# Performance work log

Measured on AMD Instinct MI355X. Metric: run time of the kernel, lower is better.

## Reference

```python
import jax, jax.numpy as jnp
import numpy as np

SCALE = 8      # scale_factor from map_to_mat_info
PATCH = 32     # up_delta - low_delta + 1 == right_delta - left_delta + 1 (uniform interior patches)


def setup_inputs() -> dict:
    key = jax.random.key(0)
    mat_h, mat_w = 160, 160
    H = (mat_h - 1) * SCALE + PATCH  # 1304: deltas (0,31,0,31) -> no border clipping
    W = (mat_w - 1) * SCALE + PATCH
    x = jax.random.normal(key, (1, 3, H, W), dtype=jnp.float32)
    rgb_weight = jnp.array([0.299, 0.587, 0.114], dtype=jnp.float32).reshape(1, 3, 1, 1)
    return {"x": x, "rgb_weight": rgb_weight, "mat_h": mat_h, "mat_w": mat_w}


def reference(x, rgb_weight, mat_h, mat_w):
    P = PATCH
    # RGB -> grayscale (convert_gray branch for in_channels == 3)
    gray = jnp.sum(x * rgb_weight, axis=1)[0]  # (H, W)
    # Gather all overlapping PxP patches at stride SCALE -> (mat_h, mat_w, P, P)
    rows = (jnp.arange(mat_h) * SCALE)[:, None] + jnp.arange(P)[None, :]  # (mat_h, P)
    cols = (jnp.arange(mat_w) * SCALE)[:, None] + jnp.arange(P)[None, :]  # (mat_w, P)
    p = gray[rows.reshape(-1)].reshape(mat_h, P, -1)              # (mat_h, P, W)
    p = p[:, :, cols.reshape(-1)].reshape(mat_h, P, mat_w, P)     # (mat_h, P, mat_w, P)
    patches = jnp.transpose(p, (0, 2, 1, 3))                      # (mat_h, mat_w, P, P)
    # torch.rfft(signal_ndim=2, onesided=False) == full 2D FFT; power = re^2 + im^2
    F = jnp.fft.fft2(patches)
    log_power = jnp.log(F.real * F.real + F.imag * F.imag + 1.0)
    # High-frequency region sums (h == w == P, static)
    lo = P // 2 - P // 4 - 1   # 7
    up = P // 2 + P // 4       # 24
    r1 = jnp.sum(log_power[..., lo:up + 1, :], axis=(-2, -1))
    r2 = jnp.sum(log_power[..., up + 1:, lo:up + 1], axis=(-2, -1))
    r3 = jnp.sum(log_power[..., :lo, lo:up + 1], axis=(-2, -1))
    mat = (r1 + r2 + r3)[None, None]  # (1, 1, mat_h, mat_w)
    return mat / jnp.max(mat)
```

## Files before the change

### kernel.cpp

```cpp
#include <hip/hip_runtime.h>
#include <math.h>

#define SCALE 8
#define PSZ 32

#define RSTRIDE 92
#define SSTRIDE (17 * RSTRIDE)

__device__ constexpr float C32[16] = {
     1.000000000000000f,  0.980785280403230f,  0.923879532511287f,  0.831469612302545f,
     0.707106781186548f,  0.555570233019602f,  0.382683432365090f,  0.195090322016128f,
     0.000000000000000f, -0.195090322016128f, -0.382683432365090f, -0.555570233019602f,
    -0.707106781186548f, -0.831469612302545f, -0.923879532511287f, -0.980785280403230f };
__device__ constexpr float S32[16] = {
     0.000000000000000f,  0.195090322016128f,  0.382683432365090f,  0.555570233019602f,
     0.707106781186548f,  0.831469612302545f,  0.923879532511287f,  0.980785280403230f,
     1.000000000000000f,  0.980785280403230f,  0.923879532511287f,  0.831469612302545f,
     0.707106781186548f,  0.555570233019602f,  0.382683432365090f,  0.195090322016128f };

__device__ __forceinline__ constexpr int brev4(int i) {
    return ((i & 1) << 3) | ((i & 2) << 1) | ((i & 4) >> 1) | ((i & 8) >> 3);
}

__device__ __forceinline__ void fft16(float re[16], float im[16]) {
#pragma unroll
    for (int i = 0; i < 16; ++i) {
        const int j = brev4(i);
        if (j > i) {
            float t = re[i]; re[i] = re[j]; re[j] = t;
            t = im[i]; im[i] = im[j]; im[j] = t;
        }
    }
#pragma unroll
    for (int s = 1; s <= 4; ++s) {
        const int m = 1 << s;
        const int h = m >> 1;
        const int tstep = 32 >> s;
#pragma unroll
        for (int k = 0; k < 16; k += m) {
#pragma unroll
            for (int j = 0; j < h; ++j) {
                const float wr = C32[j * tstep];
                const float wi = -S32[j * tstep];
                const int a = k + j;
                const int b = k + j + h;
                const float tr = wr * re[b] - wi * im[b];
                const float ti = wr * im[b] + wi * re[b];
                re[b] = re[a] - tr; im[b] = im[a] - ti;
                re[a] = re[a] + tr; im[a] = im[a] + ti;
            }
        }
    }
}

__device__ __forceinline__ unsigned pack_bf2(float hi, float lo) {
    const unsigned uh = __float_as_uint(hi) + 0x8000u;
    const unsigned ul = __float_as_uint(lo) + 0x8000u;
    return (uh & 0xFFFF0000u) | (ul >> 16);
}
__device__ __forceinline__ float bf_hi(unsigned u) { return __uint_as_float(u & 0xFFFF0000u); }
__device__ __forceinline__ float bf_lo(unsigned u) { return __uint_as_float(u << 16); }

__global__ __launch_bounds__(256) void gray_kernel(
        const float* __restrict__ x, const float* __restrict__ w,
        float* __restrict__ g, int n4, long long HW) {
    const int i = blockIdx.x * 256 + threadIdx.x;
    if (i >= n4) return;
    const float w0 = w[0], w1 = w[1], w2 = w[2];
    const float4 a = reinterpret_cast<const float4*>(x)[i];
    const float4 b = reinterpret_cast<const float4*>(x + HW)[i];
    const float4 c = reinterpret_cast<const float4*>(x + 2 * HW)[i];
    float4 o;
    o.x = w0 * a.x + w1 * b.x + w2 * c.x;
    o.y = w0 * a.y + w1 * b.y + w2 * c.y;
    o.z = w0 * a.z + w1 * b.z + w2 * c.z;
    o.w = w0 * a.w + w1 * b.w + w2 * c.w;
    reinterpret_cast<float4*>(g)[i] = o;
}

__global__ __launch_bounds__(256) void hfdft_tile_kernel(
        const float* __restrict__ g, float* __restrict__ out,
        float* __restrict__ partial, int W, int mat_w) {
    __shared__ unsigned spec[2 * SSTRIDE];
    __shared__ float red[16];

    const int tid = threadIdx.x;
    const int row0 = blockIdx.y * 64;
    const int col0 = blockIdx.x * 16;

    const bool is_even = (tid < 88);
    const bool is_odd = (tid >= 128 && tid < 216);
    if (is_even || is_odd) {
        const int y = is_even ? tid : (tid - 128);
        const float4* g4 = reinterpret_cast<const float4*>(
            g + (size_t)(row0 + y) * W + col0);
        float win[40];
#pragma unroll
        for (int q = 0; q < 10; ++q) {
            const float4 v = g4[q];
            win[4 * q + 0] = v.x; win[4 * q + 1] = v.y;
            win[4 * q + 2] = v.z; win[4 * q + 3] = v.w;
        }

        unsigned* sA = spec + y;
        unsigned* sB = spec + SSTRIDE + y;

        float fr[16], fi[16];
        if (is_even) {
#pragma unroll
            for (int i = 0; i < 16; ++i) {
                fr[i] = win[i] + win[i + 16];
                fi[i] = win[i + 8] + win[i + 24];
            }
            fft16(fr, fi);
            sA[0] = pack_bf2(fr[0], fr[8]);
            sB[0] = pack_bf2(fi[0], fi[8]);
#pragma unroll
            for (int k2 = 1; k2 <= 7; ++k2) {
                const int e2 = 16 - k2;
                const float far_ = 0.5f * (fr[k2] + fr[e2]);
                const float fai_ = 0.5f * (fi[k2] - fi[e2]);
                const float fbr_ = 0.5f * (fi[k2] + fi[e2]);
                const float fbi_ = 0.5f * (fr[e2] - fr[k2]);
                sA[(2 * k2) * RSTRIDE] = pack_bf2(far_, fai_);
                sB[(2 * k2) * RSTRIDE] = pack_bf2(fbr_, fbi_);
            }
        } else {
#pragma unroll
            for (int i = 0; i < 16; ++i) {
                const float dre = win[i] - win[i + 16];
                const float dim = win[i + 8] - win[i + 24];
                fr[i] = dre * C32[i] + dim * S32[i];
                fi[i] = dim * C32[i] - dre * S32[i];
            }
            fft16(fr, fi);
#pragma unroll
            for (int k2 = 0; k2 <= 7; ++k2) {
                const int o2 = 15 - k2;
                const float far_ = 0.5f * (fr[k2] + fr[o2]);
                const float fai_ = 0.5f * (fi[k2] - fi[o2]);
                const float fbr_ = 0.5f * (fi[k2] + fi[o2]);
                const float fbi_ = 0.5f * (fr[o2] - fr[k2]);
                sA[(2 * k2 + 1) * RSTRIDE] = pack_bf2(far_, fai_);
                sB[(2 * k2 + 1) * RSTRIDE] = pack_bf2(fbr_, fbi_);
            }
        }
    }

    __syncthreads();

    {
        const int pl = tid >> 4;
        const int slot = tid & 15;
        const int ph = pl >> 1, strip = pl & 1;
        const float b1f = (slot >= 7) ? 1.0f : 0.0f;
        const float m1f = (slot >= 8) ? 1.0f : 0.0f;

        unsigned u[32];
        {
            const uint4* p4 = reinterpret_cast<const uint4*>(
                spec + strip * SSTRIDE + slot * RSTRIDE + ph * 8);
#pragma unroll
            for (int q = 0; q < 8; ++q) {
                const uint4 v = p4[q];
                u[4 * q + 0] = v.x; u[4 * q + 1] = v.y;
                u[4 * q + 2] = v.z; u[4 * q + 3] = v.w;
            }
        }

        float s0 = 0.0f, s1 = 0.0f;

        {
            float er[16], ei[16];
#pragma unroll
            for (int i = 0; i < 16; ++i) {
                er[i] = bf_hi(u[i]) + bf_hi(u[i + 16]);
                ei[i] = bf_lo(u[i]) + bf_lo(u[i + 16]);
            }
            fft16(er, ei);
            if (slot == 0) {
#pragma unroll
                for (int k2 = 0; k2 <= 8; ++k2) {
                    const int kr = 2 * k2;
                    const int b = (k2 == 0) ? 0 : 16 - k2;
                    const float g0r = 0.5f * (er[k2] + er[b]);
                    const float g0i = 0.5f * (ei[k2] - ei[b]);
                    const float g1r = 0.5f * (ei[k2] + ei[b]);
                    const float g1i = 0.5f * (er[b] - er[k2]);
                    const float w0c = (kr >= 7 ? 1.0f : 0.0f) + ((kr >= 8 && kr <= 15) ? 1.0f : 0.0f);
                    const float w16c = 1.0f + ((kr >= 1 && kr <= 15) ? 1.0f : 0.0f);
                    if (w0c > 0.0f)
                        s0 = fmaf(w0c, __logf(g0r * g0r + g0i * g0i + 1.0f), s0);
                    s1 = fmaf(w16c, __logf(g1r * g1r + g1i * g1i + 1.0f), s1);
                }
            } else {
#pragma unroll
                for (int k2 = 0; k2 < 16; ++k2) {
                    const int kr = 2 * k2;
                    const float lp = __logf(er[k2] * er[k2] + ei[k2] * ei[k2] + 1.0f);
                    const float wgt = (kr >= 8 && kr <= 24) ? 2.0f : (b1f + m1f);
                    if (k2 & 1) s1 = fmaf(wgt, lp, s1);
                    else        s0 = fmaf(wgt, lp, s0);
                }
            }
        }

        {
            float orr[16], oi[16];
#pragma unroll
            for (int i = 0; i < 16; ++i) {
                const float dre = bf_hi(u[i]) - bf_hi(u[i + 16]);
                const float dim = bf_lo(u[i]) - bf_lo(u[i + 16]);
                orr[i] = dre * C32[i] + dim * S32[i];
                oi[i]  = dim * C32[i] - dre * S32[i];
            }
            fft16(orr, oi);
            if (slot == 0) {
#pragma unroll
                for (int k2 = 0; k2 <= 7; ++k2) {
                    const int kr = 2 * k2 + 1;
                    const int b = 15 - k2;
                    const float g0r = 0.5f * (orr[k2] + orr[b]);
                    const float g0i = 0.5f * (oi[k2] - oi[b]);
                    const float g1r = 0.5f * (oi[k2] + oi[b]);
                    const float g1i = 0.5f * (orr[b] - orr[k2]);
                    const float w0c = (kr >= 7 ? 1.0f : 0.0f) + ((kr >= 8 && kr <= 15) ? 1.0f : 0.0f);
                    const float w16c = 2.0f;
                    if (w0c > 0.0f)
                        s0 = fmaf(w0c, __logf(g0r * g0r + g0i * g0i + 1.0f), s0);
                    s1 = fmaf(w16c, __logf(g1r * g1r + g1i * g1i + 1.0f), s1);
                }
            } else {
#pragma unroll
                for (int k2 = 0; k2 < 16; ++k2) {
                    const int kr = 2 * k2 + 1;
                    const float lp = __logf(orr[k2] * orr[k2] + oi[k2] * oi[k2] + 1.0f);
                    float wgt;
                    if (kr == 7)                   wgt = 1.0f + m1f;
                    else if (kr == 25)             wgt = b1f + 1.0f;
                    else if (kr >= 9 && kr <= 23)  wgt = 2.0f;
                    else                           wgt = b1f + m1f;
                    if (k2 & 1) s1 = fmaf(wgt, lp, s1);
                    else        s0 = fmaf(wgt, lp, s0);
                }
            }
        }

        float s = s0 + s1;
#pragma unroll
        for (int off = 8; off >= 1; off >>= 1) s += __shfl_xor(s, off, 16);
        if (slot == 0) {
            out[(blockIdx.y * 8 + ph) * mat_w + blockIdx.x * 2 + strip] = s;
            red[pl] = s;
        }
    }

    __syncthreads();

    if (tid == 0) {
        float m = red[0];
#pragma unroll
        for (int i = 1; i < 16; ++i) m = fmaxf(m, red[i]);
        partial[blockIdx.y * gridDim.x + blockIdx.x] = m;
    }
}

template <bool GRAY_PRE>
__global__ __launch_bounds__(128) void hfdft_patch_kernel(
        const float* __restrict__ x, const float* __restrict__ w,
        float* __restrict__ out, int H, int W, int mat_h, int mat_w) {
    __shared__ unsigned cb[4 * 528];
    __shared__ float red[8];

    const int tid = threadIdx.x;
    const int h = tid >> 6;
    const int lane = tid & 63;
    const int total = mat_h * mat_w;
    const long long HW = (long long)H * W;
    const int Pbase = blockIdx.x * 4;

    {
        const int g = lane >> 5, r = lane & 31;
        int pA = Pbase + 2 * g;
        if (pA > total - 1) pA = total - 1;
        int pB = pA + 1; if (pB > total - 1) pB = total - 1;
        const int phA = pA / mat_w, pwA = pA % mat_w;
        const int phB = pB / mat_w, pwB = pB % mat_w;
        const bool adj = (phA == phB) && (pwB == pwA + 1);
        const int baseA = (phA * SCALE + r) * W + pwA * SCALE;
        const int baseB = (phB * SCALE + r) * W + pwB * SCALE;

        float ar[32], br[32];
        if (GRAY_PRE && adj) {
            float win[40];
            const float4* g4 = reinterpret_cast<const float4*>(x + baseA);
#pragma unroll
            for (int q = 0; q < 10; ++q) {
                const float4 v = g4[q];
                win[4 * q + 0] = v.x; win[4 * q + 1] = v.y;
                win[4 * q + 2] = v.z; win[4 * q + 3] = v.w;
            }
#pragma unroll
            for (int i = 0; i < 32; ++i) { ar[i] = win[i]; br[i] = win[i + 8]; }
        } else if (GRAY_PRE) {
#pragma unroll
            for (int i = 0; i < 32; ++i) { ar[i] = x[baseA + i]; br[i] = x[baseB + i]; }
        } else {
            const float w0 = w[0], w1 = w[1], w2 = w[2];
#pragma unroll
            for (int i = 0; i < 32; ++i) {
                ar[i] = w0 * x[baseA + i] + w1 * x[HW + baseA + i] + w2 * x[2 * HW + baseA + i];
                br[i] = w0 * x[baseB + i] + w1 * x[HW + baseB + i] + w2 * x[2 * HW + baseB + i];
            }
        }

        float fr[16], fi[16];
        if (h == 0) {
#pragma unroll
            for (int i = 0; i < 16; ++i) {
                fr[i] = ar[i] + ar[i + 16];
                fi[i] = br[i] + br[i + 16];
            }
        } else {
#pragma unroll
            for (int i = 0; i < 16; ++i) {
                const float dre = ar[i] - ar[i + 16];
                const float dim = br[i] - br[i + 16];
                fr[i] = dre * C32[i] + dim * S32[i];
                fi[i] = dim * C32[i] - dre * S32[i];
            }
        }

        fft16(fr, fi);

        unsigned* cbA = cb + (2 * g) * 528;
        unsigned* cbB = cbA + 528;
        if (h == 0) {
            cbA[r] = pack_bf2(fr[0], fr[8]);
            cbB[r] = pack_bf2(fi[0], fi[8]);
#pragma unroll
            for (int k2 = 1; k2 <= 7; ++k2) {
                const int e2 = 16 - k2;
                const float far_ = 0.5f * (fr[k2] + fr[e2]);
                const float fai_ = 0.5f * (fi[k2] - fi[e2]);
                const float fbr_ = 0.5f * (fi[k2] + fi[e2]);
                const float fbi_ = 0.5f * (fr[e2] - fr[k2]);
                cbA[(2 * k2) * 33 + r] = pack_bf2(far_, fai_);
                cbB[(2 * k2) * 33 + r] = pack_bf2(fbr_, fbi_);
            }
        } else {
#pragma unroll
            for (int k2 = 0; k2 <= 7; ++k2) {
                const int o2 = 15 - k2;
                const float far_ = 0.5f * (fr[k2] + fr[o2]);
                const float fai_ = 0.5f * (fi[k2] - fi[o2]);
                const float fbr_ = 0.5f * (fi[k2] + fi[o2]);
                const float fbi_ = 0.5f * (fr[o2] - fr[k2]);
                cbA[(2 * k2 + 1) * 33 + r] = pack_bf2(far_, fai_);
                cbB[(2 * k2 + 1) * 33 + r] = pack_bf2(fbr_, fbi_);
            }
        }
    }

    __syncthreads();

    {
        const int pl = lane >> 4, slot = lane & 15;
        int p = Pbase + pl;
        if (p > total - 1) p = total - 1;
        const unsigned* cbp = cb + pl * 528 + slot * 33;

        float fr[16], fi[16];
        if (h == 0) {
#pragma unroll
            for (int i = 0; i < 16; ++i) {
                const unsigned u0 = cbp[i], u1 = cbp[i + 16];
                fr[i] = bf_hi(u0) + bf_hi(u1);
                fi[i] = bf_lo(u0) + bf_lo(u1);
            }
        } else {
#pragma unroll
            for (int i = 0; i < 16; ++i) {
                const unsigned u0 = cbp[i], u1 = cbp[i + 16];
                const float dre = bf_hi(u0) - bf_hi(u1);
                const float dim = bf_lo(u0) - bf_lo(u1);
                fr[i] = dre * C32[i] + dim * S32[i];
                fi[i] = dim * C32[i] - dre * S32[i];
            }
        }

        fft16(fr, fi);

        float s0 = 0.0f, s1 = 0.0f;
        if (slot == 0) {
            if (h == 0) {
#pragma unroll
                for (int k2 = 0; k2 <= 8; ++k2) {
                    const int kr = 2 * k2;
                    const int b = (k2 == 0) ? 0 : 16 - k2;
                    const float g0r = 0.5f * (fr[k2] + fr[b]);
                    const float g0i = 0.5f * (fi[k2] - fi[b]);
                    const float g1r = 0.5f * (fi[k2] + fi[b]);
                    const float g1i = 0.5f * (fr[b] - fr[k2]);
                    const float w0c = (kr >= 7 ? 1.0f : 0.0f) + ((kr >= 8 && kr <= 15) ? 1.0f : 0.0f);
                    const float w16c = 1.0f + ((kr >= 1 && kr <= 15) ? 1.0f : 0.0f);
                    if (w0c > 0.0f)
                        s0 = fmaf(w0c, __logf(g0r * g0r + g0i * g0i + 1.0f), s0);
                    s1 = fmaf(w16c, __logf(g1r * g1r + g1i * g1i + 1.0f), s1);
                }
            } else {
#pragma unroll
                for (int k2 = 0; k2 <= 7; ++k2) {
                    const int kr = 2 * k2 + 1;
                    const int b = 15 - k2;
                    const float g0r = 0.5f * (fr[k2] + fr[b]);
                    const float g0i = 0.5f * (fi[k2] - fi[b]);
                    const float g1r = 0.5f * (fi[k2] + fi[b]);
                    const float g1i = 0.5f * (fr[b] - fr[k2]);
                    const float w0c = (kr >= 7 ? 1.0f : 0.0f) + ((kr >= 8 && kr <= 15) ? 1.0f : 0.0f);
                    const float w16c = 2.0f;
                    if (w0c > 0.0f)
                        s0 = fmaf(w0c, __logf(g0r * g0r + g0i * g0i + 1.0f), s0);
                    s1 = fmaf(w16c, __logf(g1r * g1r + g1i * g1i + 1.0f), s1);
                }
            }
        } else {
            const float b1f = (slot >= 7) ? 1.0f : 0.0f;
            const float m1f = (slot >= 8) ? 1.0f : 0.0f;
            if (h == 0) {
#pragma unroll
                for (int k2 = 0; k2 < 16; ++k2) {
                    const int kr = 2 * k2;
                    const float lp = __logf(fr[k2] * fr[k2] + fi[k2] * fi[k2] + 1.0f);
                    const float wgt = (kr >= 8 && kr <= 24) ? 2.0f : (b1f + m1f);
                    if (k2 & 1) s1 = fmaf(wgt, lp, s1);
                    else        s0 = fmaf(wgt, lp, s0);
                }
            } else {
#pragma unroll
                for (int k2 = 0; k2 < 16; ++k2) {
                    const int kr = 2 * k2 + 1;
                    const float lp = __logf(fr[k2] * fr[k2] + fi[k2] * fi[k2] + 1.0f);
                    float wgt;
                    if (kr == 7)                   wgt = 1.0f + m1f;
                    else if (kr == 25)             wgt = b1f + 1.0f;
                    else if (kr >= 9 && kr <= 23)  wgt = 2.0f;
                    else                           wgt = b1f + m1f;
                    if (k2 & 1) s1 = fmaf(wgt, lp, s1);
                    else        s0 = fmaf(wgt, lp, s0);
                }
            }
        }

        float s = s0 + s1;
#pragma unroll
        for (int off = 8; off >= 1; off >>= 1) s += __shfl_xor(s, off, 16);
        if (slot == 0) red[pl * 2 + h] = s;
    }

    __syncthreads();

    if (tid < 4) {
        const int p = Pbase + tid;
        if (p < total) out[p] = red[tid * 2] + red[tid * 2 + 1];
    }
}

__global__ __launch_bounds__(1024) void max_kernel(
        const float* __restrict__ sums, int n, float* __restrict__ partial) {
    __shared__ float sm[16];
    float m = 0.0f;
    for (int i = blockIdx.x * 1024 + threadIdx.x; i < n; i += gridDim.x * 1024)
        m = fmaxf(m, sums[i]);
#pragma unroll
    for (int off = 32; off >= 1; off >>= 1) m = fmaxf(m, __shfl_xor(m, off, 64));
    if ((threadIdx.x & 63) == 0) sm[threadIdx.x >> 6] = m;
    __syncthreads();
    if (threadIdx.x == 0) {
#pragma unroll
        for (int i = 1; i < 16; ++i) m = fmaxf(m, sm[i]);
        partial[blockIdx.x] = m;
    }
}

__global__ __launch_bounds__(256) void norm_kernel(
        float* __restrict__ out, int n,
        const float* __restrict__ partial, int np) {
    __shared__ float sm[4];
    float m = 0.0f;
    for (int i = threadIdx.x; i < np; i += 256) m = fmaxf(m, partial[i]);
#pragma unroll
    for (int off = 32; off >= 1; off >>= 1) m = fmaxf(m, __shfl_xor(m, off, 64));
    if ((threadIdx.x & 63) == 0) sm[threadIdx.x >> 6] = m;
    __syncthreads();
    m = fmaxf(fmaxf(sm[0], sm[1]), fmaxf(sm[2], sm[3]));
    const int i = blockIdx.x * 256 + threadIdx.x;
    if (i < n) out[i] = out[i] / m;
}

extern "C" void kernel_launch(void* const* d_in, const int* in_sizes, int n_in,
                              void* d_out, int out_size, void* d_ws, size_t ws_size,
                              hipStream_t stream) {
    const float* x = (const float*)d_in[0];
    const float* w = (const float*)d_in[1];
    float* out = (float*)d_out;

    const int HWi = in_sizes[0] / 3;
    const int H = (int)(sqrt((double)HWi) + 0.5);
    const int W = H;
    const long long HW = (long long)H * W;
    const int mat = (int)(sqrt((double)out_size) + 0.5);
    const int total = mat * mat;

    float* partial = (float*)d_ws;
    float* gray = (float*)((char*)d_ws + 8192);
    const int nparts = (mat / 2) * (mat / 8);
    const size_t need = 8192 + (size_t)HW * 4;

    const bool shape_ok = ((mat & 7) == 0) && (W == (mat - 1) * SCALE + PSZ)
                          && (H == W) && ((W & 3) == 0)
                          && ws_size >= need && (size_t)nparts * 4 <= 8192;

    if (shape_ok) {
        const int n4 = (int)(HW / 4);
        hipLaunchKernelGGL(gray_kernel, dim3((n4 + 255) / 256), dim3(256), 0, stream,
                           x, w, gray, n4, HW);
        dim3 gridT(mat / 2, mat / 8);
        hipLaunchKernelGGL(hfdft_tile_kernel, gridT, dim3(256), 0, stream,
                           gray, out, partial, W, mat);
        hipLaunchKernelGGL(norm_kernel, dim3((total + 255) / 256), dim3(256), 0, stream,
                           out, total, partial, nparts);
    } else if (ws_size >= need && (W & 3) == 0) {
        const int n4 = (int)(HW / 4);
        hipLaunchKernelGGL(gray_kernel, dim3((n4 + 255) / 256), dim3(256), 0, stream,
                           x, w, gray, n4, HW);
        hipLaunchKernelGGL((hfdft_patch_kernel<true>), dim3((total + 3) / 4), dim3(128), 0, stream,
                           gray, w, out, H, W, mat, mat);
        hipLaunchKernelGGL(max_kernel, dim3(8), dim3(1024), 0, stream, out, total, partial);
        hipLaunchKernelGGL(norm_kernel, dim3((total + 255) / 256), dim3(256), 0, stream,
                           out, total, partial, 8);
    } else {
        hipLaunchKernelGGL((hfdft_patch_kernel<false>), dim3((total + 3) / 4), dim3(128), 0, stream,
                           x, w, out, H, W, mat, mat);
        hipLaunchKernelGGL(max_kernel, dim3(8), dim3(1024), 0, stream, out, total, partial);
        hipLaunchKernelGGL(norm_kernel, dim3((total + 255) / 256), dim3(256), 0, stream,
                           out, total, partial, 8);
    }
}
```

Before: 43.71 us.

## Fuse grayscale conversion into tile kernel via shared-memory window staging

```diff
diff --git a/kernel.cpp b/kernel.cpp
--- a/kernel.cpp
+++ b/kernel.cpp
@@ -4,6 +4,7 @@
 #define SCALE 8
 #define PSZ 32
 
+#define WSTRIDE 41
 #define RSTRIDE 92
 #define SSTRIDE (17 * RSTRIDE)
 
@@ -60,6 +61,212 @@
 }
 __device__ __forceinline__ float bf_hi(unsigned u) { return __uint_as_float(u & 0xFFFF0000u); }
 __device__ __forceinline__ float bf_lo(unsigned u) { return __uint_as_float(u << 16); }
+
+__global__ __launch_bounds__(256) void hfdft_tile_kernel(
+        const float* __restrict__ x, const float* __restrict__ w,
+        float* __restrict__ out, float* __restrict__ partial,
+        int W, int mat_w, long long HW) {
+    __shared__ float win[88 * WSTRIDE];
+    __shared__ unsigned spec[2 * SSTRIDE];
+    __shared__ float red[16];
+
+    const int tid = threadIdx.x;
+    const int row0 = blockIdx.y * 64;
+    const int col0 = blockIdx.x * 16;
+
+    {
+        const float w0 = w[0], w1 = w[1], w2 = w[2];
+        for (int idx = tid; idx < 880; idx += 256) {
+            const int row = idx / 10;
+            const int f4 = idx - row * 10;
+            const float* base = x + (size_t)(row0 + row) * W + col0 + f4 * 4;
+            const float4 a = *reinterpret_cast<const float4*>(base);
+            const float4 b = *reinterpret_cast<const float4*>(base + HW);
+            const float4 c = *reinterpret_cast<const float4*>(base + 2 * HW);
+            float* wp = win + row * WSTRIDE + f4 * 4;
+            wp[0] = w0 * a.x + w1 * b.x + w2 * c.x;
+            wp[1] = w0 * a.y + w1 * b.y + w2 * c.y;
+            wp[2] = w0 * a.z + w1 * b.z + w2 * c.z;
+            wp[3] = w0 * a.w + w1 * b.w + w2 * c.w;
+        }
+    }
+
+    __syncthreads();
+
+    const bool is_even = (tid < 88);
+    const bool is_odd = (tid >= 128 && tid < 216);
+    if (is_even || is_odd) {
+        const int y = is_even ? tid : (tid - 128);
+        const float* wrow = win + y * WSTRIDE;
+
+        unsigned* sA = spec + y;
+        unsigned* sB = spec + SSTRIDE + y;
+
+        float fr[16], fi[16];
+        if (is_even) {
+#pragma unroll
+            for (int i = 0; i < 16; ++i) {
+                fr[i] = wrow[i] + wrow[i + 16];
+                fi[i] = wrow[i + 8] + wrow[i + 24];
+            }
+            fft16(fr, fi);
+            sA[0] = pack_bf2(fr[0], fr[8]);
+            sB[0] = pack_bf2(fi[0], fi[8]);
+#pragma unroll
+            for (int k2 = 1; k2 <= 7; ++k2) {
+                const int e2 = 16 - k2;
+                const float far_ = 0.5f * (fr[k2] + fr[e2]);
+                const float fai_ = 0.5f * (fi[k2] - fi[e2]);
+                const float fbr_ = 0.5f * (fi[k2] + fi[e2]);
+                const float fbi_ = 0.5f * (fr[e2] - fr[k2]);
+                sA[(2 * k2) * RSTRIDE] = pack_bf2(far_, fai_);
+                sB[(2 * k2) * RSTRIDE] = pack_bf2(fbr_, fbi_);
+            }
+        } else {
+#pragma unroll
+            for (int i = 0; i < 16; ++i) {
+                const float dre = wrow[i] - wrow[i + 16];
+                const float dim = wrow[i + 8] - wrow[i + 24];
+                fr[i] = dre * C32[i] + dim * S32[i];
+                fi[i] = dim * C32[i] - dre * S32[i];
+            }
+            fft16(fr, fi);
+#pragma unroll
+            for (int k2 = 0; k2 <= 7; ++k2) {
+                const int o2 = 15 - k2;
+                const float far_ = 0.5f * (fr[k2] + fr[o2]);
+                const float fai_ = 0.5f * (fi[k2] - fi[o2]);
+                const float fbr_ = 0.5f * (fi[k2] + fi[o2]);
+                const float fbi_ = 0.5f * (fr[o2] - fr[k2]);
+                sA[(2 * k2 + 1) * RSTRIDE] = pack_bf2(far_, fai_);
+                sB[(2 * k2 + 1) * RSTRIDE] = pack_bf2(fbr_, fbi_);
+            }
+        }
+    }
+
+    __syncthreads();
+
+    {
+        const int pl = tid >> 4;
+        const int slot = tid & 15;
+        const int ph = pl >> 1, strip = pl & 1;
+        const uint4* p4 = reinterpret_cast<const uint4*>(
+            spec + strip * SSTRIDE + slot * RSTRIDE + ph * 8);
+        const float b1f = (slot >= 7) ? 1.0f : 0.0f;
+        const float m1f = (slot >= 8) ? 1.0f : 0.0f;
+
+        float s0 = 0.0f, s1 = 0.0f;
+
+        {
+            float er[16], ei[16];
+#pragma unroll
+            for (int q = 0; q < 4; ++q) {
+                const uint4 lo = p4[q];
+                const uint4 hi = p4[q + 4];
+                er[4 * q + 0] = bf_hi(lo.x) + bf_hi(hi.x);
+                ei[4 * q + 0] = bf_lo(lo.x) + bf_lo(hi.x);
+                er[4 * q + 1] = bf_hi(lo.y) + bf_hi(hi.y);
+                ei[4 * q + 1] = bf_lo(lo.y) + bf_lo(hi.y);
+                er[4 * q + 2] = bf_hi(lo.z) + bf_hi(hi.z);
+                ei[4 * q + 2] = bf_lo(lo.z) + bf_lo(hi.z);
+                er[4 * q + 3] = bf_hi(lo.w) + bf_hi(hi.w);
+                ei[4 * q + 3] = bf_lo(lo.w) + bf_lo(hi.w);
+            }
+            fft16(er, ei);
+            if (slot == 0) {
+#pragma unroll
+                for (int k2 = 0; k2 <= 8; ++k2) {
+                    const int kr = 2 * k2;
+                    const int b = (k2 == 0) ? 0 : 16 - k2;
+                    const float g0r = 0.5f * (er[k2] + er[b]);
+                    const float g0i = 0.5f * (ei[k2] - ei[b]);
+                    const float g1r = 0.5f * (ei[k2] + ei[b]);
+                    const float g1i = 0.5f * (er[b] - er[k2]);
+                    const float w0c = (kr >= 7 ? 1.0f : 0.0f) + ((kr >= 8 && kr <= 15) ? 1.0f : 0.0f);
+                    const float w16c = 1.0f + ((kr >= 1 && kr <= 15) ? 1.0f : 0.0f);
+                    if (w0c > 0.0f)
+                        s0 = fmaf(w0c, __logf(g0r * g0r + g0i * g0i + 1.0f), s0);
+                    s1 = fmaf(w16c, __logf(g1r * g1r + g1i * g1i + 1.0f), s1);
+                }
+            } else {
+#pragma unroll
+                for (int k2 = 0; k2 < 16; ++k2) {
+                    const int kr = 2 * k2;
+                    const float lp = __logf(er[k2] * er[k2] + ei[k2] * ei[k2] + 1.0f);
+                    const float wgt = (kr >= 8 && kr <= 24) ? 2.0f : (b1f + m1f);
+                    if (k2 & 1) s1 = fmaf(wgt, lp, s1);
+                    else        s0 = fmaf(wgt, lp, s0);
+                }
+            }
+        }
+
+        {
+            float orr[16], oi[16];
+#pragma unroll
+            for (int q = 0; q < 4; ++q) {
+                const uint4 lo = p4[q];
+                const uint4 hi = p4[q + 4];
+#pragma unroll
+                for (int j = 0; j < 4; ++j) {
+                    const unsigned ul = (&lo.x)[j];
+                    const unsigned uh = (&hi.x)[j];
+                    const int i = 4 * q + j;
+                    const float dre = bf_hi(ul) - bf_hi(uh);
+                    const float dim = bf_lo(ul) - bf_lo(uh);
+                    orr[i] = dre * C32[i] + dim * S32[i];
+                    oi[i]  = dim * C32[i] - dre * S32[i];
+                }
+            }
+            fft16(orr, oi);
+            if (slot == 0) {
+#pragma unroll
+                for (int k2 = 0; k2 <= 7; ++k2) {
+                    const int kr = 2 * k2 + 1;
+                    const int b = 15 - k2;
+                    const float g0r = 0.5f * (orr[k2] + orr[b]);
+                    const float g0i = 0.5f * (oi[k2] - oi[b]);
+                    const float g1r = 0.5f * (oi[k2] + oi[b]);
+                    const float g1i = 0.5f * (orr[b] - orr[k2]);
+                    const float w0c = (kr >= 7 ? 1.0f : 0.0f) + ((kr >= 8 && kr <= 15) ? 1.0f : 0.0f);
+                    const float w16c = 2.0f;
+                    if (w0c > 0.0f)
+                        s0 = fmaf(w0c, __logf(g0r * g0r + g0i * g0i + 1.0f), s0);
+                    s1 = fmaf(w16c, __logf(g1r * g1r + g1i * g1i + 1.0f), s1);
+                }
+            } else {
+#pragma unroll
+                for (int k2 = 0; k2 < 16; ++k2) {
+                    const int kr = 2 * k2 + 1;
+                    const float lp = __logf(orr[k2] * orr[k2] + oi[k2] * oi[k2] + 1.0f);
+                    float wgt;
+                    if (kr == 7)                   wgt = 1.0f + m1f;
+                    else if (kr == 25)             wgt = b1f + 1.0f;
+                    else if (kr >= 9 && kr <= 23)  wgt = 2.0f;
+                    else                           wgt = b1f + m1f;
+                    if (k2 & 1) s1 = fmaf(wgt, lp, s1);
+                    else        s0 = fmaf(wgt, lp, s0);
+                }
+            }
+        }
+
+        float s = s0 + s1;
+#pragma unroll
+        for (int off = 8; off >= 1; off >>= 1) s += __shfl_xor(s, off, 16);
+        if (slot == 0) {
+            out[(blockIdx.y * 8 + ph) * mat_w + blockIdx.x * 2 + strip] = s;
+            red[pl] = s;
+        }
+    }
+
+    __syncthreads();
+
+    if (tid == 0) {
+        float m = red[0];
+#pragma unroll
+        for (int i = 1; i < 16; ++i) m = fmaxf(m, red[i]);
+        partial[blockIdx.y * gridDim.x + blockIdx.x] = m;
+    }
+}
 
 __global__ __launch_bounds__(256) void gray_kernel(
         const float* __restrict__ x, const float* __restrict__ w,
@@ -78,193 +285,6 @@
     reinterpret_cast<float4*>(g)[i] = o;
 }
 
-__global__ __launch_bounds__(256) void hfdft_tile_kernel(
-        const float* __restrict__ g, float* __restrict__ out,
-        float* __restrict__ partial, int W, int mat_w) {
-    __shared__ unsigned spec[2 * SSTRIDE];
-    __shared__ float red[16];
-
-    const int tid = threadIdx.x;
-    const int row0 = blockIdx.y * 64;
-    const int col0 = blockIdx.x * 16;
-
-    const bool is_even = (tid < 88);
-    const bool is_odd = (tid >= 128 && tid < 216);
-    if (is_even || is_odd) {
-        const int y = is_even ? tid : (tid - 128);
-        const float4* g4 = reinterpret_cast<const float4*>(
-            g + (size_t)(row0 + y) * W + col0);
-        float win[40];
-#pragma unroll
-        for (int q = 0; q < 10; ++q) {
-            const float4 v = g4[q];
-            win[4 * q + 0] = v.x; win[4 * q + 1] = v.y;
-            win[4 * q + 2] = v.z; win[4 * q + 3] = v.w;
-        }
-
-        unsigned* sA = spec + y;
-        unsigned* sB = spec + SSTRIDE + y;
-
-        float fr[16], fi[16];
-        if (is_even) {
-#pragma unroll
-            for (int i = 0; i < 16; ++i) {
-                fr[i] = win[i] + win[i + 16];
-                fi[i] = win[i + 8] + win[i + 24];
-            }
-            fft16(fr, fi);
-            sA[0] = pack_bf2(fr[0], fr[8]);
-            sB[0] = pack_bf2(fi[0], fi[8]);
-#pragma unroll
-            for (int k2 = 1; k2 <= 7; ++k2) {
-                const int e2 = 16 - k2;
-                const float far_ = 0.5f * (fr[k2] + fr[e2]);
-                const float fai_ = 0.5f * (fi[k2] - fi[e2]);
-                const float fbr_ = 0.5f * (fi[k2] + fi[e2]);
-                const float fbi_ = 0.5f * (fr[e2] - fr[k2]);
-                sA[(2 * k2) * RSTRIDE] = pack_bf2(far_, fai_);
-                sB[(2 * k2) * RSTRIDE] = pack_bf2(fbr_, fbi_);
-            }
-        } else {
-#pragma unroll
-            for (int i = 0; i < 16; ++i) {
-                const float dre = win[i] - win[i + 16];
-                const float dim = win[i + 8] - win[i + 24];
-                fr[i] = dre * C32[i] + dim * S32[i];
-                fi[i] = dim * C32[i] - dre * S32[i];
-            }
-            fft16(fr, fi);
-#pragma unroll
-            for (int k2 = 0; k2 <= 7; ++k2) {
-                const int o2 = 15 - k2;
-                const float far_ = 0.5f * (fr[k2] + fr[o2]);
-                const float fai_ = 0.5f * (fi[k2] - fi[o2]);
-                const float fbr_ = 0.5f * (fi[k2] + fi[o2]);
-                const float fbi_ = 0.5f * (fr[o2] - fr[k2]);
-                sA[(2 * k2 + 1) * RSTRIDE] = pack_bf2(far_, fai_);
-                sB[(2 * k2 + 1) * RSTRIDE] = pack_bf2(fbr_, fbi_);
-            }
-        }
-    }
-
-    __syncthreads();
-
-    {
-        const int pl = tid >> 4;
-        const int slot = tid & 15;
-        const int ph = pl >> 1, strip = pl & 1;
-        const float b1f = (slot >= 7) ? 1.0f : 0.0f;
-        const float m1f = (slot >= 8) ? 1.0f : 0.0f;
-
-        unsigned u[32];
-        {
-            const uint4* p4 = reinterpret_cast<const uint4*>(
-                spec + strip * SSTRIDE + slot * RSTRIDE + ph * 8);
-#pragma unroll
-            for (int q = 0; q < 8; ++q) {
-                const uint4 v = p4[q];
-                u[4 * q + 0] = v.x; u[4 * q + 1] = v.y;
-                u[4 * q + 2] = v.z; u[4 * q + 3] = v.w;
-            }
-        }
-
-        float s0 = 0.0f, s1 = 0.0f;
-
-        {
-            float er[16], ei[16];
-#pragma unroll
-            for (int i = 0; i < 16; ++i) {
-                er[i] = bf_hi(u[i]) + bf_hi(u[i + 16]);
-                ei[i] = bf_lo(u[i]) + bf_lo(u[i + 16]);
-            }
-            fft16(er, ei);
-            if (slot == 0) {
-#pragma unroll
-                for (int k2 = 0; k2 <= 8; ++k2) {
-                    const int kr = 2 * k2;
-                    const int b = (k2 == 0) ? 0 : 16 - k2;
-                    const float g0r = 0.5f * (er[k2] + er[b]);
-                    const float g0i = 0.5f * (ei[k2] - ei[b]);
-                    const float g1r = 0.5f * (ei[k2] + ei[b]);
-                    const float g1i = 0.5f * (er[b] - er[k2]);
-                    const float w0c = (kr >= 7 ? 1.0f : 0.0f) + ((kr >= 8 && kr <= 15) ? 1.0f : 0.0f);
-                    const float w16c = 1.0f + ((kr >= 1 && kr <= 15) ? 1.0f : 0.0f);
-                    if (w0c > 0.0f)
-                        s0 = fmaf(w0c, __logf(g0r * g0r + g0i * g0i + 1.0f), s0);
-                    s1 = fmaf(w16c, __logf(g1r * g1r + g1i * g1i + 1.0f), s1);
-                }
-            } else {
-#pragma unroll
-                for (int k2 = 0; k2 < 16; ++k2) {
-                    const int kr = 2 * k2;
-                    const float lp = __logf(er[k2] * er[k2] + ei[k2] * ei[k2] + 1.0f);
-                    const float wgt = (kr >= 8 && kr <= 24) ? 2.0f : (b1f + m1f);
-                    if (k2 & 1) s1 = fmaf(wgt, lp, s1);
-                    else        s0 = fmaf(wgt, lp, s0);
-                }
-            }
-        }
-
-        {
-            float orr[16], oi[16];
-#pragma unroll
-            for (int i = 0; i < 16; ++i) {
-                const float dre = bf_hi(u[i]) - bf_hi(u[i + 16]);
-                const float dim = bf_lo(u[i]) - bf_lo(u[i + 16]);
-                orr[i] = dre * C32[i] + dim * S32[i];
-                oi[i]  = dim * C32[i] - dre * S32[i];
-            }
-            fft16(orr, oi);
-            if (slot == 0) {
-#pragma unroll
-                for (int k2 = 0; k2 <= 7; ++k2) {
-                    const int kr = 2 * k2 + 1;
-                    const int b = 15 - k2;
-                    const float g0r = 0.5f * (orr[k2] + orr[b]);
-                    const float g0i = 0.5f * (oi[k2] - oi[b]);
-                    const float g1r = 0.5f * (oi[k2] + oi[b]);
-                    const float g1i = 0.5f * (orr[b] - orr[k2]);
-                    const float w0c = (kr >= 7 ? 1.0f : 0.0f) + ((kr >= 8 && kr <= 15) ? 1.0f : 0.0f);
-                    const float w16c = 2.0f;
-                    if (w0c > 0.0f)
-                        s0 = fmaf(w0c, __logf(g0r * g0r + g0i * g0i + 1.0f), s0);
-                    s1 = fmaf(w16c, __logf(g1r * g1r + g1i * g1i + 1.0f), s1);
-                }
-            } else {
-#pragma unroll
-                for (int k2 = 0; k2 < 16; ++k2) {
-                    const int kr = 2 * k2 + 1;
-                    const float lp = __logf(orr[k2] * orr[k2] + oi[k2] * oi[k2] + 1.0f);
-                    float wgt;
-                    if (kr == 7)                   wgt = 1.0f + m1f;
-                    else if (kr == 25)             wgt = b1f + 1.0f;
-                    else if (kr >= 9 && kr <= 23)  wgt = 2.0f;
-                    else                           wgt = b1f + m1f;
-                    if (k2 & 1) s1 = fmaf(wgt, lp, s1);
-                    else        s0 = fmaf(wgt, lp, s0);
-                }
-            }
-        }
-
-        float s = s0 + s1;
-#pragma unroll
-        for (int off = 8; off >= 1; off >>= 1) s += __shfl_xor(s, off, 16);
-        if (slot == 0) {
-            out[(blockIdx.y * 8 + ph) * mat_w + blockIdx.x * 2 + strip] = s;
-            red[pl] = s;
-        }
-    }
-
-    __syncthreads();
-
-    if (tid == 0) {
-        float m = red[0];
-#pragma unroll
-        for (int i = 1; i < 16; ++i) m = fmaxf(m, red[i]);
-        partial[blockIdx.y * gridDim.x + blockIdx.x] = m;
-    }
-}
-
 template <bool GRAY_PRE>
 __global__ __launch_bounds__(128) void hfdft_patch_kernel(
         const float* __restrict__ x, const float* __restrict__ w,
@@ -292,16 +312,16 @@
 
         float ar[32], br[32];
         if (GRAY_PRE && adj) {
-            float win[40];
+            float win2[40];
             const float4* g4 = reinterpret_cast<const float4*>(x + baseA);
 #pragma unroll
             for (int q = 0; q < 10; ++q) {
                 const float4 v = g4[q];
-                win[4 * q + 0] = v.x; win[4 * q + 1] = v.y;
-                win[4 * q + 2] = v.z; win[4 * q + 3] = v.w;
-            }
-#pragma unroll
-            for (int i = 0; i < 32; ++i) { ar[i] = win[i]; br[i] = win[i + 8]; }
+                win2[4 * q + 0] = v.x; win2[4 * q + 1] = v.y;
+                win2[4 * q + 2] = v.z; win2[4 * q + 3] = v.w;
+            }
+#pragma unroll
+            for (int i = 0; i < 32; ++i) { ar[i] = win2[i]; br[i] = win2[i + 8]; }
         } else if (GRAY_PRE) {
 #pragma unroll
             for (int i = 0; i < 32; ++i) { ar[i] = x[baseA + i]; br[i] = x[baseB + i]; }
@@ -515,22 +535,19 @@
     float* partial = (float*)d_ws;
     float* gray = (float*)((char*)d_ws + 8192);
     const int nparts = (mat / 2) * (mat / 8);
-    const size_t need = 8192 + (size_t)HW * 4;
+    const size_t need_fb = 8192 + (size_t)HW * 4;
 
     const bool shape_ok = ((mat & 7) == 0) && (W == (mat - 1) * SCALE + PSZ)
                           && (H == W) && ((W & 3) == 0)
-                          && ws_size >= need && (size_t)nparts * 4 <= 8192;
+                          && ws_size >= (size_t)nparts * 4;
 
     if (shape_ok) {
-        const int n4 = (int)(HW / 4);
-        hipLaunchKernelGGL(gray_kernel, dim3((n4 + 255) / 256), dim3(256), 0, stream,
-                           x, w, gray, n4, HW);
         dim3 gridT(mat / 2, mat / 8);
         hipLaunchKernelGGL(hfdft_tile_kernel, gridT, dim3(256), 0, stream,
-                           gray, out, partial, W, mat);
+                           x, w, out, partial, W, mat, HW);
         hipLaunchKernelGGL(norm_kernel, dim3((total + 255) / 256), dim3(256), 0, stream,
                            out, total, partial, nparts);
-    } else if (ws_size >= need && (W & 3) == 0) {
+    } else if (ws_size >= need_fb && (W & 3) == 0) {
         const int n4 = (int)(HW / 4);
         hipLaunchKernelGGL(gray_kernel, dim3((n4 + 255) / 256), dim3(256), 0, stream,
                            x, w, gray, n4, HW);
```

After: 45.29 us. 1.04x slower.
